# Kernel optimization log

Hardware: AMD Instinct MI355X
Metric: run time of the kernel (lower is better)

Reference implementation:

```python
import jax, jax.numpy as jnp
import numpy as np

DIM = 128
HEADS = 8
DH = DIM // HEADS
WIN = (4, 4, 4)
TOPK = 4
EPS = 1e-6


def _ln(x, g, b):
    mu = jnp.mean(x, -1, keepdims=True)
    var = jnp.mean((x - mu) ** 2, -1, keepdims=True)
    return (x - mu) * jax.lax.rsqrt(var + EPS) * g + b


def _win3d(x, p1, p2, p3):
    # x: [B,S,H,W,C] -> [B, p1*p2*p3, Ms, Mh, Mw, C]
    B, S, H, W, C = x.shape
    Ms, Mh, Mw = S // p1, H // p2, W // p3
    x = x.reshape(B, p1, Ms, p2, Mh, p3, Mw, C)
    x = x.transpose(0, 1, 3, 5, 2, 4, 6, 7)
    return x.reshape(B, p1 * p2 * p3, Ms, Mh, Mw, C)


def setup_inputs() -> dict:
    key = jax.random.key(0)
    ks = jax.random.split(key, 20)

    def lin(k, din, dout):
        return jax.random.normal(k, (din, dout), jnp.float32) * 0.02

    return {
        "x_in": jax.random.normal(ks[0], (2, 128, 16, 32, 32), jnp.float32),
        "x_g_in": jax.random.normal(ks[1], (2, 128, 8, 16, 16), jnp.float32),
        # Atten (global branch)
        "qkv_w": lin(ks[2], DIM, 3 * DIM), "qkv_b": jnp.zeros((3 * DIM,), jnp.float32),
        "proj_w": lin(ks[3], DIM, DIM), "proj_b": jnp.zeros((DIM,), jnp.float32),
        # shared LayerNorm (self.norm1 is reused everywhere in the original)
        "ln_g": jnp.ones((DIM,), jnp.float32), "ln_b": jnp.zeros((DIM,), jnp.float32),
        # mlp (global branch FFN)
        "mlp_w1": lin(ks[4], DIM, 4 * DIM), "mlp_b1": jnp.zeros((4 * DIM,), jnp.float32),
        "mlp_w2": lin(ks[5], 4 * DIM, DIM), "mlp_b2": jnp.zeros((DIM,), jnp.float32),
        # TopkRouting
        "rq_w": lin(ks[6], DIM, DIM), "rq_b": jnp.zeros((DIM,), jnp.float32),
        "rk_w": lin(ks[7], DIM, DIM), "rk_b": jnp.zeros((DIM,), jnp.float32),
        # fused qkv over concatenated local+gathered-global tokens
        "gqkv_w": lin(ks[8], DIM, 3 * DIM), "gqkv_b": jnp.zeros((3 * DIM,), jnp.float32),
        "wo_w": lin(ks[9], DIM, DIM), "wo_b": jnp.zeros((DIM,), jnp.float32),
        # mlp2 (local branch FFN)
        "mlp2_w1": lin(ks[10], DIM, 4 * DIM), "mlp2_b1": jnp.zeros((4 * DIM,), jnp.float32),
        "mlp2_w2": lin(ks[11], 4 * DIM, DIM), "mlp2_b2": jnp.zeros((DIM,), jnp.float32),
    }


def reference(x_in, x_g_in, qkv_w, qkv_b, proj_w, proj_b, ln_g, ln_b,
              mlp_w1, mlp_b1, mlp_w2, mlp_b2, rq_w, rq_b, rk_w, rk_b,
              gqkv_w, gqkv_b, wo_w, wo_b, mlp2_w1, mlp2_b1, mlp2_w2, mlp2_b2):
    B, C, S, H, W = x_in.shape
    Ms, Mh, Mw = WIN
    p1, p2, p3 = S // Ms, H // Mh, W // Mw  # pads are zero for these shapes
    nw, w3l = p1 * p2 * p3, Ms * Mh * Mw
    scale = DIM ** -0.5  # BiLevelRoutingAttention.scale = dim**-0.5 (not per-head)

    x = jnp.transpose(x_in, (0, 2, 3, 4, 1))  # [B,S,H,W,C]
    shortcut_l = _win3d(x, p1, p2, p3).reshape(B, nw, w3l, C)

    # ---- global branch: full self-attention + FFN ----
    _, _, gS, gH, gW = x_g_in.shape
    gN = gS * gH * gW
    xg = jnp.transpose(x_g_in, (0, 2, 3, 4, 1)).reshape(B, gN, C)
    h = _ln(xg, ln_g, ln_b)
    qkv = (h @ qkv_w + qkv_b).reshape(B, gN, 3, HEADS, DH).transpose(2, 0, 3, 1, 4)
    q, k, v = qkv[0], qkv[1], qkv[2]
    a = jax.nn.softmax(jnp.einsum('bhnd,bhmd->bhnm', q, k) * DH ** -0.5, axis=-1)
    o = jnp.einsum('bhnm,bhmd->bhnd', a, v).transpose(0, 2, 1, 3).reshape(B, gN, C)
    xg = (o @ proj_w + proj_b) + xg
    xg4 = xg.reshape(B, gS, gH, gW, C)
    h = _ln(xg4, ln_g, ln_b)
    xg4 = xg4 + (jax.nn.gelu(h @ mlp_w1 + mlp_b1, approximate=False) @ mlp_w2 + mlp_b2)

    # ---- top-k window routing ----
    swg = _win3d(xg4, p1, p2, p3)  # [B,nw,gMs,gMh,gMw,C]
    w3g = swg.shape[2] * swg.shape[3] * swg.shape[4]
    g_win = swg.mean((2, 3, 4))  # [B,nw,C]
    qh = g_win @ rq_w + rq_b
    kh = g_win @ rk_w + rk_b
    logit = jnp.einsum('bnc,bmc->bnm', qh * scale, kh)
    _tvals, tidx = jax.lax.top_k(logit, TOPK)  # r_weight is computed but unused in the original forward

    # gather top-k global windows' tokens per local window
    gflat = swg.reshape(B, nw, w3g, C)
    gath = jax.vmap(lambda kv, idx: kv[idx])(gflat, tidx)  # [B,nw,topk,w3g,C]
    sc = jnp.concatenate([shortcut_l, gath.reshape(B, nw, TOPK * w3g, C)], axis=2)
    w3 = w3l + TOPK * w3g

    # ---- local+routed attention over concatenated tokens ----
    qkvp = _ln(sc, ln_g, ln_b) @ gqkv_w + gqkv_b
    qp, kp, vp = jnp.split(qkvp, 3, axis=-1)
    qp = qp.reshape(B, nw, w3, HEADS, DH)
    kp = kp.reshape(B, nw, w3, HEADS, DH)
    vp = vp.reshape(B, nw, w3, HEADS, DH)
    aw = jax.nn.softmax(jnp.einsum('bnqhd,bnkhd->bnhqk', qp * scale, kp), axis=-1)
    out = jnp.einsum('bnhqk,bnkhd->bnqhd', aw, vp).reshape(B, nw, w3, C)

    l = out[:, :, :w3l] @ wo_w + wo_b + shortcut_l
    l = l.reshape(B, p1, p2, p3, Ms, Mh, Mw, C).transpose(0, 1, 4, 2, 5, 3, 6, 7).reshape(B, S, H, W, C)
    l = l + (jax.nn.gelu(_ln(l, ln_g, ln_b) @ mlp2_w1 + mlp2_b1, approximate=False) @ mlp2_w2 + mlp2_b2)

    l_out = jnp.transpose(l, (0, 4, 1, 2, 3))
    g_out = jnp.transpose(xg4, (0, 4, 1, 2, 3))
    return (l_out, g_out)
```

## Files before the change

### kernel.cpp

```cpp
#include <hip/hip_runtime.h>
#include <hip/hip_bf16.h>
#include <math.h>

#define BATCH 2
#define CDIM 128
#define SS 16
#define HH_ 32
#define WW_ 32
#define NSP (SS*HH_*WW_)
#define GS 8
#define GH 16
#define GW 16
#define GN (GS*GH*GW)
#define HEADS 8
#define DH 16
#define NW 256
#define W3L 64
#define W3G 8
#define TOPK 4
#define W3 (W3L + TOPK*W3G)
#define LN_EPS 1e-6f
#define ROUTE_SCALE 0.08838834764831845f
#define GATTN_SCALE 0.25f

typedef short bshort8 __attribute__((ext_vector_type(8)));
typedef float f32x4 __attribute__((ext_vector_type(4)));

__device__ __forceinline__ unsigned short f2bf(float f) {
    unsigned int u = __float_as_uint(f);
    unsigned int r = (u + 0x7fffu + ((u >> 16) & 1u)) >> 16;
    return (unsigned short)r;
}
__device__ __forceinline__ float gelu_exact(float x) {
    return 0.5f * x * (1.0f + erff(x * 0.70710678118654752f));
}
__device__ __forceinline__ float shfl_sum32(float v) {
#pragma unroll
    for (int m = 16; m > 0; m >>= 1) v += __shfl_xor(v, m);
    return v;
}
__device__ __forceinline__ float shfl_sum16(float v) {
#pragma unroll
    for (int m = 8; m > 0; m >>= 1) v += __shfl_xor(v, m);
    return v;
}
__device__ __forceinline__ float shfl_sum8(float v) {
#pragma unroll
    for (int m = 4; m > 0; m >>= 1) v += __shfl_xor(v, m);
    return v;
}

__global__ __launch_bounds__(256) void k_wprep_all(const float* __restrict__ gqkv_w,
        const float* __restrict__ m2_w1, const float* __restrict__ m2_w2,
        const float* __restrict__ proj_w, const float* __restrict__ mlp_w1,
        const float* __restrict__ mlp_w2, const float* __restrict__ wo_w,
        const float* __restrict__ qkv_w,
        unsigned short* __restrict__ wt, unsigned short* __restrict__ w1t,
        unsigned short* __restrict__ w2t, unsigned short* __restrict__ projt,
        unsigned short* __restrict__ gw1t, unsigned short* __restrict__ gw2t,
        unsigned short* __restrict__ wot, unsigned short* __restrict__ qkvt) {
    int id = blockIdx.x * 256 + threadIdx.x;
    if (id < 49152) {
        int n = id >> 7, k = id & 127;
        float v = gqkv_w[k * 384 + n];
        if (n < 128) v *= ROUTE_SCALE;
        wt[id] = f2bf(v);
    } else if (id < 114688) {
        int i = id - 49152; int n = i >> 7, k = i & 127;
        w1t[i] = f2bf(m2_w1[k * 512 + n]);
    } else if (id < 180224) {
        int i = id - 114688; int n = i >> 9, k = i & 511;
        w2t[i] = f2bf(m2_w2[k * 128 + n]);
    } else if (id < 196608) {
        int i = id - 180224; int n = i >> 7, k = i & 127;
        projt[i] = f2bf(proj_w[k * 128 + n]);
    } else if (id < 262144) {
        int i = id - 196608; int n = i >> 7, k = i & 127;
        gw1t[i] = f2bf(mlp_w1[k * 512 + n]);
    } else if (id < 327680) {
        int i = id - 262144; int n = i >> 9, k = i & 511;
        gw2t[i] = f2bf(mlp_w2[k * 128 + n]);
    } else if (id < 344064) {
        int i = id - 327680; int n = i >> 7, k = i & 127;
        wot[i] = f2bf(wo_w[k * 128 + n]);
    } else {
        int i = id - 344064; int n = i >> 7, k = i & 127;
        float v = qkv_w[k * 384 + n];
        if (n < 128) v *= GATTN_SCALE;
        qkvt[i] = f2bf(v);
    }
}

__global__ __launch_bounds__(256) void k_gqkv_mfma(const float* __restrict__ xg_in,
        const unsigned short* __restrict__ qkvt, const float* __restrict__ qkv_b,
        const float* __restrict__ ln_g, const float* __restrict__ ln_b,
        float* __restrict__ xg, unsigned short* __restrict__ qgb,
        unsigned short* __restrict__ kgb, unsigned short* __restrict__ vgtb) {
    int blk = blockIdx.x; int b = blk >> 7; int n0 = (blk & 127) * 16;
    int t = threadIdx.x; int w = t >> 6; int lane = t & 63;
    int l15 = lane & 15, quad = lane >> 4;
    __shared__ __align__(16) float xs[16 * 132];
    __shared__ __align__(16) unsigned short h[16 * 136];
    f32x4 zero4 = {0.f, 0.f, 0.f, 0.f};

    {
        int c = t >> 1, j0 = (t & 1) * 8;
        const float* src = xg_in + ((size_t)(b * 128 + c)) * GN + n0 + j0;
        float4 v0 = *(const float4*)src;
        float4 v1 = *(const float4*)(src + 4);
        xs[(j0 + 0) * 132 + c] = v0.x; xs[(j0 + 1) * 132 + c] = v0.y;
        xs[(j0 + 2) * 132 + c] = v0.z; xs[(j0 + 3) * 132 + c] = v0.w;
        xs[(j0 + 4) * 132 + c] = v1.x; xs[(j0 + 5) * 132 + c] = v1.y;
        xs[(j0 + 6) * 132 + c] = v1.z; xs[(j0 + 7) * 132 + c] = v1.w;
    }
    __syncthreads();
    {
        int j = t >> 4, p = t & 15, c0 = p * 8;
        float vv[8]; float s1 = 0.f;
#pragma unroll
        for (int i = 0; i < 8; i++) { vv[i] = xs[j * 132 + c0 + i]; s1 += vv[i]; }
        s1 = shfl_sum16(s1);
        float mu = s1 * (1.0f / 128.0f);
        float s2 = 0.f;
#pragma unroll
        for (int i = 0; i < 8; i++) { float d = vv[i] - mu; s2 += d * d; }
        s2 = shfl_sum16(s2);
        float rs = rsqrtf(s2 * (1.0f / 128.0f) + LN_EPS);
        float* dst = xg + ((size_t)(b * GN) + n0 + j) * 128 + c0;
        *(float4*)dst = *(float4*)&vv[0];
        *(float4*)(dst + 4) = *(float4*)&vv[4];
        unsigned short hb[8];
#pragma unroll
        for (int i4 = 0; i4 < 2; i4++) {
            float4 g4 = *(const float4*)(ln_g + c0 + i4 * 4);
            float4 b4 = *(const float4*)(ln_b + c0 + i4 * 4);
            hb[i4 * 4 + 0] = f2bf((vv[i4 * 4 + 0] - mu) * rs * g4.x + b4.x);
            hb[i4 * 4 + 1] = f2bf((vv[i4 * 4 + 1] - mu) * rs * g4.y + b4.y);
            hb[i4 * 4 + 2] = f2bf((vv[i4 * 4 + 2] - mu) * rs * g4.z + b4.z);
            hb[i4 * 4 + 3] = f2bf((vv[i4 * 4 + 3] - mu) * rs * g4.w + b4.w);
        }
        *(ushort4*)&h[j * 136 + c0] = *(ushort4*)&hb[0];
        *(ushort4*)&h[j * 136 + c0 + 4] = *(ushort4*)&hb[4];
    }
    __syncthreads();

    bshort8 a[4];
#pragma unroll
    for (int ks = 0; ks < 4; ks++)
        a[ks] = *(const bshort8*)(h + l15 * 136 + ks * 32 + quad * 8);
    int bh_base = b * HEADS;
#pragma unroll
    for (int part = 0; part < 2; part++) {
#pragma unroll
        for (int which = 0; which < 2; which++) {
            int nt = 2 * w + which;
            int ncol = part * 128 + nt * 16;
            f32x4 acc = zero4;
#pragma unroll
            for (int ks = 0; ks < 4; ks++) {
                bshort8 bfr = *(const bshort8*)(qkvt + (size_t)(ncol + l15) * 128 + ks * 32 + quad * 8);
                acc = __builtin_amdgcn_mfma_f32_16x16x32_bf16(a[ks], bfr, acc, 0, 0, 0);
            }
            float bias = qkv_b[ncol + l15] * (part == 0 ? GATTN_SCALE : 1.f);
            unsigned short* dst = (part == 0) ? qgb : kgb;
#pragma unroll
            for (int r = 0; r < 4; r++)
                dst[((size_t)(bh_base + nt) * GN + n0 + quad * 4 + r) * DH + l15] = f2bf(acc[r] + bias);
        }
    }
#pragma unroll
    for (int which = 0; which < 2; which++) {
        int mtv = 2 * w + which;
        f32x4 acc = zero4;
#pragma unroll
        for (int ks = 0; ks < 4; ks++) {
            bshort8 aw = *(const bshort8*)(qkvt + (size_t)(256 + mtv * 16 + l15) * 128 + ks * 32 + quad * 8);
            acc = __builtin_amdgcn_mfma_f32_16x16x32_bf16(aw, a[ks], acc, 0, 0, 0);
        }
#pragma unroll
        for (int r = 0; r < 4; r++) {
            float bias = qkv_b[256 + mtv * 16 + quad * 4 + r];
            vgtb[((size_t)(bh_base + mtv) * DH + quad * 4 + r) * GN + n0 + l15] = f2bf(acc[r] + bias);
        }
    }
}

__global__ __launch_bounds__(256) void k_gattn_mfma(const unsigned short* __restrict__ qgb,
        const unsigned short* __restrict__ kgb, const unsigned short* __restrict__ vgtb,
        float* __restrict__ og) {
    int blk = blockIdx.x;
    int bh = blk >> 7; int qt = (blk & 127) << 4;
    int b = bh >> 3, hh = bh & 7;
    int t = threadIdx.x; int w = t >> 6; int lane = t & 63;
    int col = lane & 15, quad = lane >> 4;
    __shared__ __align__(16) unsigned short Pbuf[4 * 16 * 40];
    __shared__ float po[4][64][4];
    __shared__ float pl[4][64][4];

    bshort8 aq = {0, 0, 0, 0, 0, 0, 0, 0};
    if (quad < 2)
        aq = *(const bshort8*)(qgb + ((size_t)bh * GN + qt + col) * DH + quad * 8);

    f32x4 o = {0.f, 0.f, 0.f, 0.f};
    float lsum[4] = {0.f, 0.f, 0.f, 0.f};
    const unsigned short* kb = kgb + (size_t)bh * GN * DH;
    const unsigned short* vb = vgtb + (size_t)bh * DH * GN;
    unsigned short* pb = Pbuf + w * (16 * 40);
    int row0 = quad * 4;
    int kbeg = w * 512;
    for (int kc = kbeg; kc < kbeg + 512; kc += 32) {
        bshort8 bk0 = {0, 0, 0, 0, 0, 0, 0, 0};
        bshort8 bk1 = {0, 0, 0, 0, 0, 0, 0, 0};
        if (quad < 2) {
            bk0 = *(const bshort8*)(kb + (size_t)(kc + col) * DH + quad * 8);
            bk1 = *(const bshort8*)(kb + (size_t)(kc + 16 + col) * DH + quad * 8);
        }
        f32x4 z = {0.f, 0.f, 0.f, 0.f};
        f32x4 s0 = __builtin_amdgcn_mfma_f32_16x16x32_bf16(aq, bk0, z, 0, 0, 0);
        f32x4 s1 = __builtin_amdgcn_mfma_f32_16x16x32_bf16(aq, bk1, z, 0, 0, 0);
        float p0[4], p1[4];
#pragma unroll
        for (int r = 0; r < 4; r++) {
            p0[r] = __expf(s0[r]); p1[r] = __expf(s1[r]);
            lsum[r] += p0[r] + p1[r];
        }
#pragma unroll
        for (int r = 0; r < 4; r++) {
            pb[(row0 + r) * 40 + col] = f2bf(p0[r]);
            pb[(row0 + r) * 40 + 16 + col] = f2bf(p1[r]);
        }
        bshort8 pA = *(const bshort8*)(pb + col * 40 + quad * 8);
        bshort8 bv = *(const bshort8*)(vb + (size_t)col * GN + kc + quad * 8);
        o = __builtin_amdgcn_mfma_f32_16x16x32_bf16(pA, bv, o, 0, 0, 0);
    }
#pragma unroll
    for (int r = 0; r < 4; r++) {
        float v = lsum[r];
        v += __shfl_xor(v, 1); v += __shfl_xor(v, 2);
        v += __shfl_xor(v, 4); v += __shfl_xor(v, 8);
        lsum[r] = v;
    }
#pragma unroll
    for (int r = 0; r < 4; r++) { po[w][lane][r] = o[r]; pl[w][lane][r] = lsum[r]; }
    __syncthreads();
    if (w == 0) {
#pragma unroll
        for (int r = 0; r < 4; r++) {
            float os = po[0][lane][r] + po[1][lane][r] + po[2][lane][r] + po[3][lane][r];
            float ls = pl[0][lane][r] + pl[1][lane][r] + pl[2][lane][r] + pl[3][lane][r];
            og[((size_t)(b * GN) + qt + quad * 4 + r) * 128 + hh * 16 + col] = os / ls;
        }
    }
}

__global__ __launch_bounds__(256) void k_gmlp_mfma(const float* __restrict__ og,
        const float* __restrict__ xg,
        const unsigned short* __restrict__ projt, const float* __restrict__ proj_b,
        const float* __restrict__ ln_g, const float* __restrict__ ln_b,
        const unsigned short* __restrict__ gw1t, const float* __restrict__ b1,
        const unsigned short* __restrict__ gw2t, const float* __restrict__ b2,
        float* __restrict__ xg4, float* __restrict__ gout) {
    int blk = blockIdx.x; int b = blk >> 7; int n0g = (blk & 127) * 16;
    int t = threadIdx.x; int w = t >> 6; int lane = t & 63;
    int l15 = lane & 15, quad = lane >> 4;
    __shared__ __align__(16) unsigned short ao[16 * 136];
    __shared__ __align__(16) float xs[16 * 132];
    __shared__ __align__(16) unsigned short h[16 * 136];
    __shared__ __align__(16) unsigned short h1[16 * 520];
    float* of32 = (float*)h1;
    f32x4 zero4 = {0.f, 0.f, 0.f, 0.f};

    {
        int j = t >> 4, p = t & 15, c0 = p * 8;
        size_t base = ((size_t)(b * GN) + n0g + j) * 128 + c0;
        float4 v0 = *(const float4*)(og + base);
        float4 v1 = *(const float4*)(og + base + 4);
        ushort4 u0 = { f2bf(v0.x), f2bf(v0.y), f2bf(v0.z), f2bf(v0.w) };
        ushort4 u1 = { f2bf(v1.x), f2bf(v1.y), f2bf(v1.z), f2bf(v1.w) };
        *(ushort4*)&ao[j * 136 + c0] = u0;
        *(ushort4*)&ao[j * 136 + c0 + 4] = u1;
        *(float4*)&xs[j * 132 + c0] = *(const float4*)(xg + base);
        *(float4*)&xs[j * 132 + c0 + 4] = *(const float4*)(xg + base + 4);
    }
    __syncthreads();

    {
        bshort8 a[4];
#pragma unroll
        for (int ks = 0; ks < 4; ks++)
            a[ks] = *(const bshort8*)(ao + l15 * 136 + ks * 32 + quad * 8);
#pragma unroll
        for (int nt = 0; nt < 2; nt++) {
            int n0 = w * 32 + nt * 16;
            f32x4 acc = zero4;
#pragma unroll
            for (int ks = 0; ks < 4; ks++) {
                bshort8 bfr = *(const bshort8*)(projt + (n0 + l15) * 128 + ks * 32 + quad * 8);
                acc = __builtin_amdgcn_mfma_f32_16x16x32_bf16(a[ks], bfr, acc, 0, 0, 0);
            }
            float bias = proj_b[n0 + l15];
#pragma unroll
            for (int r = 0; r < 4; r++) {
                int m = quad * 4 + r;
                xs[m * 132 + n0 + l15] += acc[r] + bias;
            }
        }
    }
    __syncthreads();

    {
        int j = t >> 4, p = t & 15, c0 = p * 8;
        float vv[8]; float s1 = 0.f;
#pragma unroll
        for (int i = 0; i < 8; i++) { vv[i] = xs[j * 132 + c0 + i]; s1 += vv[i]; }
        s1 = shfl_sum16(s1);
        float mu = s1 * (1.0f / 128.0f);
        float s2 = 0.f;
#pragma unroll
        for (int i = 0; i < 8; i++) { float d = vv[i] - mu; s2 += d * d; }
        s2 = shfl_sum16(s2);
        float rs = rsqrtf(s2 * (1.0f / 128.0f) + LN_EPS);
        unsigned short hb[8];
#pragma unroll
        for (int i4 = 0; i4 < 2; i4++) {
            float4 g4 = *(const float4*)(ln_g + c0 + i4 * 4);
            float4 b4 = *(const float4*)(ln_b + c0 + i4 * 4);
            hb[i4 * 4 + 0] = f2bf((vv[i4 * 4 + 0] - mu) * rs * g4.x + b4.x);
            hb[i4 * 4 + 1] = f2bf((vv[i4 * 4 + 1] - mu) * rs * g4.y + b4.y);
            hb[i4 * 4 + 2] = f2bf((vv[i4 * 4 + 2] - mu) * rs * g4.z + b4.z);
            hb[i4 * 4 + 3] = f2bf((vv[i4 * 4 + 3] - mu) * rs * g4.w + b4.w);
        }
        *(ushort4*)&h[j * 136 + c0] = *(ushort4*)&hb[0];
        *(ushort4*)&h[j * 136 + c0 + 4] = *(ushort4*)&hb[4];
    }
    __syncthreads();

    {
        bshort8 a[4];
#pragma unroll
        for (int ks = 0; ks < 4; ks++)
            a[ks] = *(const bshort8*)(h + l15 * 136 + ks * 32 + quad * 8);
#pragma unroll
        for (int nt = 0; nt < 8; nt++) {
            int n0 = w * 128 + nt * 16;
            f32x4 acc = zero4;
#pragma unroll
            for (int ks = 0; ks < 4; ks++) {
                bshort8 bfr = *(const bshort8*)(gw1t + (size_t)(n0 + l15) * 128 + ks * 32 + quad * 8);
                acc = __builtin_amdgcn_mfma_f32_16x16x32_bf16(a[ks], bfr, acc, 0, 0, 0);
            }
            float bias = b1[n0 + l15];
#pragma unroll
            for (int r = 0; r < 4; r++)
                h1[(quad * 4 + r) * 520 + n0 + l15] = f2bf(gelu_exact(acc[r] + bias));
        }
    }
    __syncthreads();

    f32x4 acc2[2]; acc2[0] = zero4; acc2[1] = zero4;
#pragma unroll 4
    for (int ks = 0; ks < 16; ks++) {
        bshort8 a = *(const bshort8*)(h1 + l15 * 520 + ks * 32 + quad * 8);
#pragma unroll
        for (int nt = 0; nt < 2; nt++) {
            int n0 = w * 32 + nt * 16;
            bshort8 bfr = *(const bshort8*)(gw2t + (size_t)(n0 + l15) * 512 + ks * 32 + quad * 8);
            acc2[nt] = __builtin_amdgcn_mfma_f32_16x16x32_bf16(a, bfr, acc2[nt], 0, 0, 0);
        }
    }
    __syncthreads();

    {
#pragma unroll
        for (int nt = 0; nt < 2; nt++) {
            int n0 = w * 32 + nt * 16;
            float bias = b2[n0 + l15];
#pragma unroll
            for (int r = 0; r < 4; r++) {
                int m = quad * 4 + r;
                float ov = xs[m * 132 + n0 + l15] + acc2[nt][r] + bias;
                of32[m * 132 + n0 + l15] = ov;
                xg4[((size_t)(b * GN) + n0g + m) * 128 + n0 + l15] = ov;
            }
        }
    }
    __syncthreads();

    {
        int cw = t >> 1, hf = t & 1, j0 = hf * 8;
        float* dst = gout + ((size_t)(b * 128 + cw)) * GN + n0g + j0;
#pragma unroll
        for (int i4 = 0; i4 < 2; i4++) {
            float4 ov = { of32[(j0 + i4 * 4 + 0) * 132 + cw], of32[(j0 + i4 * 4 + 1) * 132 + cw],
                          of32[(j0 + i4 * 4 + 2) * 132 + cw], of32[(j0 + i4 * 4 + 3) * 132 + cw] };
            *(float4*)(dst + i4 * 4) = ov;
        }
    }
}

__global__ void k_routing_qk(const float* __restrict__ xg4,
                             const float* __restrict__ rq_w, const float* __restrict__ rq_b,
                             const float* __restrict__ rk_w, const float* __restrict__ rk_b,
                             float* __restrict__ qh, float* __restrict__ kh) {
    int wid = blockIdx.x; int b = wid / NW, n = wid % NW;
    int c = threadIdx.x;
    int i1 = n / 64, i2 = (n / 8) % 8, i3 = n % 8;
    __shared__ float g[CDIM];
    float s = 0.f;
#pragma unroll
    for (int j = 0; j < W3G; j++) {
        int ds = j >> 2, dh = (j >> 1) & 1, dw = j & 1;
        int gi = ((i1 * 2 + ds) * GH + (i2 * 2 + dh)) * GW + (i3 * 2 + dw);
        s += xg4[((size_t)(b * GN + gi)) * CDIM + c];
    }
    g[c] = s * (1.0f / W3G);
    __syncthreads();
    float aq = rq_b[c], ak = rk_b[c];
    for (int k = 0; k < CDIM; k++) { float gv = g[k]; aq = fmaf(gv, rq_w[k * CDIM + c], aq); ak = fmaf(gv, rk_w[k * CDIM + c], ak); }
    qh[(size_t)wid * CDIM + c] = aq;
    kh[(size_t)wid * CDIM + c] = ak;
}

__global__ void k_topk(const float* __restrict__ qh, const float* __restrict__ kh,
                       int* __restrict__ tidx) {
    int wid = blockIdx.x; int b = wid / NW;
    int m = threadIdx.x;
    __shared__ float q[CDIM];
    __shared__ float lv[NW];
    __shared__ int li[NW];
    if (m < CDIM) q[m] = qh[(size_t)wid * CDIM + m] * ROUTE_SCALE;
    __syncthreads();
    float acc = 0.f;
    const float* kr = kh + ((size_t)b * NW + m) * CDIM;
    for (int k = 0; k < CDIM; k++) acc = fmaf(q[k], kr[k], acc);
#pragma unroll
    for (int sel = 0; sel < TOPK; sel++) {
        lv[m] = acc; li[m] = m; __syncthreads();
#pragma unroll
        for (int s = 128; s > 0; s >>= 1) {
            if (m < s) {
                if (lv[m + s] > lv[m] || (lv[m + s] == lv[m] && li[m + s] < li[m])) {
                    lv[m] = lv[m + s]; li[m] = li[m + s];
                }
            }
            __syncthreads();
        }
        int best = li[0]; __syncthreads();
        if (m == best) acc = -1e30f;
        if (m == 0) tidx[wid * TOPK + sel] = best;
    }
}

__global__ __launch_bounds__(256) void k_lnsc_local(const float* __restrict__ x_in,
        const float* __restrict__ ln_g, const float* __restrict__ ln_b,
        unsigned short* __restrict__ lnsc) {
    int blk = blockIdx.x;
    int wt = blk & 1; int hh = (blk >> 1) & 31; int s = (blk >> 6) & 15; int b = blk >> 10;
    int w0 = wt * 16;
    int t = threadIdx.x;
    __shared__ float tile[16][132];
    {
        int c = t >> 1; int wq = (t & 1) * 8;
        const float* src = x_in + (((size_t)(b * 128 + c) * SS + s)) * 1024 + hh * 32 + w0 + wq;
        float4 v0 = *(const float4*)src;
        float4 v1 = *(const float4*)(src + 4);
        tile[wq + 0][c] = v0.x; tile[wq + 1][c] = v0.y; tile[wq + 2][c] = v0.z; tile[wq + 3][c] = v0.w;
        tile[wq + 4][c] = v1.x; tile[wq + 5][c] = v1.y; tile[wq + 6][c] = v1.z; tile[wq + 7][c] = v1.w;
    }
    __syncthreads();
    int w = t >> 4; int j = t & 15;
    float vals[8];
    float s1 = 0.f;
#pragma unroll
    for (int i = 0; i < 8; i++) { vals[i] = tile[w][j * 8 + i]; s1 += vals[i]; }
    s1 = shfl_sum16(s1);
    float mu = s1 * (1.0f / 128.0f);
    float s2 = 0.f;
#pragma unroll
    for (int i = 0; i < 8; i++) { float d = vals[i] - mu; s2 += d * d; }
    s2 = shfl_sum16(s2);
    float rs = rsqrtf(s2 * (1.0f / 128.0f) + LN_EPS);
    float4 g0 = *(const float4*)(ln_g + j * 8);
    float4 g1 = *(const float4*)(ln_g + j * 8 + 4);
    float4 b0 = *(const float4*)(ln_b + j * 8);
    float4 b1 = *(const float4*)(ln_b + j * 8 + 4);
    float gv[8] = { g0.x, g0.y, g0.z, g0.w, g1.x, g1.y, g1.z, g1.w };
    float bv[8] = { b0.x, b0.y, b0.z, b0.w, b1.x, b1.y, b1.z, b1.w };
    int ww = w0 + w;
    int n = (s >> 2) * 64 + (hh >> 2) * 8 + (ww >> 2);
    int slot = (s & 3) * 16 + (hh & 3) * 4 + (ww & 3);
    unsigned short* dst = lnsc + ((size_t)(b * NW + n) * W3 + slot) * 128 + j * 8;
    ushort4 u0, u1;
    u0.x = f2bf((vals[0] - mu) * rs * gv[0] + bv[0]);
    u0.y = f2bf((vals[1] - mu) * rs * gv[1] + bv[1]);
    u0.z = f2bf((vals[2] - mu) * rs * gv[2] + bv[2]);
    u0.w = f2bf((vals[3] - mu) * rs * gv[3] + bv[3]);
    u1.x = f2bf((vals[4] - mu) * rs * gv[4] + bv[4]);
    u1.y = f2bf((vals[5] - mu) * rs * gv[5] + bv[5]);
    u1.z = f2bf((vals[6] - mu) * rs * gv[6] + bv[6]);
    u1.w = f2bf((vals[7] - mu) * rs * gv[7] + bv[7]);
    *(ushort4*)dst = u0;
    *(ushort4*)(dst + 4) = u1;
}

__global__ __launch_bounds__(256) void k_lnsc_gath(const float* __restrict__ xg4,
        const int* __restrict__ tidx,
        const float* __restrict__ ln_g, const float* __restrict__ ln_b,
        unsigned short* __restrict__ lnsc) {
    int blk = blockIdx.x;
    int kk = blk & 3; int wn = blk >> 2;
    int b = wn >> 8;
    int g = tidx[wn * TOPK + kk];
    int gi1 = g >> 6, gi2 = (g >> 3) & 7, gi3 = g & 7;
    int t = threadIdx.x; int j = t >> 5, lj = t & 31;
    int ds = j >> 2, dh = (j >> 1) & 1, dw = j & 1;
    int gi = ((gi1 * 2 + ds) * GH + (gi2 * 2 + dh)) * GW + (gi3 * 2 + dw);
    float4 v = *(const float4*)(xg4 + ((size_t)(b * GN + gi)) * 128 + lj * 4);
    float s1 = shfl_sum32(v.x + v.y + v.z + v.w);
    float mu = s1 * (1.0f / 128.0f);
    float d0 = v.x - mu, d1 = v.y - mu, d2 = v.z - mu, d3 = v.w - mu;
    float s2 = shfl_sum32(d0 * d0 + d1 * d1 + d2 * d2 + d3 * d3);
    float rs = rsqrtf(s2 * (1.0f / 128.0f) + LN_EPS);
    float4 g4 = *(const float4*)(ln_g + lj * 4);
    float4 b4 = *(const float4*)(ln_b + lj * 4);
    ushort4 u;
    u.x = f2bf(d0 * rs * g4.x + b4.x);
    u.y = f2bf(d1 * rs * g4.y + b4.y);
    u.z = f2bf(d2 * rs * g4.z + b4.z);
    u.w = f2bf(d3 * rs * g4.w + b4.w);
    *(ushort4*)(lnsc + ((size_t)wn * W3 + 64 + kk * 8 + j) * 128 + lj * 4) = u;
}

__global__ __launch_bounds__(512, 4) void k_local_mfma(const unsigned short* __restrict__ lnsc,
        const unsigned short* __restrict__ wt, const float* __restrict__ gqkv_b,
        float* __restrict__ aout) {
    int wn = blockIdx.x;
    int t = threadIdx.x; int w = t >> 6; int lane = t & 63;
    int l15 = lane & 15, quad = lane >> 4;
    __shared__ __align__(16) unsigned short Qs[64 * 136];
    __shared__ __align__(16) unsigned short Ks2[96 * 136];
    __shared__ __align__(16) unsigned short Vts[128 * 104];
    __shared__ __align__(16) unsigned short Ps[8][16 * 40];

    const unsigned short* Xb = lnsc + (size_t)wn * W3 * 128;
    f32x4 zero4 = {0.f, 0.f, 0.f, 0.f};

    bshort8 qw[4], kw[4], vw[4];
#pragma unroll
    for (int ks = 0; ks < 4; ks++) {
        qw[ks] = *(const bshort8*)(wt + (w * 16 + l15) * 128 + ks * 32 + quad * 8);
        kw[ks] = *(const bshort8*)(wt + (128 + w * 16 + l15) * 128 + ks * 32 + quad * 8);
        vw[ks] = *(const bshort8*)(wt + (256 + w * 16 + l15) * 128 + ks * 32 + quad * 8);
    }
    float qbias = gqkv_b[w * 16 + l15] * ROUTE_SCALE;
    float kbias = gqkv_b[128 + w * 16 + l15];
    float vbias[4];
#pragma unroll
    for (int r = 0; r < 4; r++) vbias[r] = gqkv_b[256 + w * 16 + quad * 4 + r];

    for (int mt = 0; mt < 6; mt++) {
        bshort8 a[4];
#pragma unroll
        for (int ks = 0; ks < 4; ks++)
            a[ks] = *(const bshort8*)(Xb + (mt * 16 + l15) * 128 + ks * 32 + quad * 8);
        f32x4 acck = zero4;
        f32x4 accv = zero4;
#pragma unroll
        for (int ks = 0; ks < 4; ks++) {
            acck = __builtin_amdgcn_mfma_f32_16x16x32_bf16(a[ks], kw[ks], acck, 0, 0, 0);
            accv = __builtin_amdgcn_mfma_f32_16x16x32_bf16(vw[ks], a[ks], accv, 0, 0, 0);
        }
#pragma unroll
        for (int r = 0; r < 4; r++) {
            Ks2[(mt * 16 + quad * 4 + r) * 136 + w * 16 + l15] = f2bf(acck[r] + kbias);
            Vts[(w * 16 + quad * 4 + r) * 104 + mt * 16 + l15] = f2bf(accv[r] + vbias[r]);
        }
        if (mt < 4) {
            f32x4 accq = zero4;
#pragma unroll
            for (int ks = 0; ks < 4; ks++)
                accq = __builtin_amdgcn_mfma_f32_16x16x32_bf16(a[ks], qw[ks], accq, 0, 0, 0);
#pragma unroll
            for (int r = 0; r < 4; r++)
                Qs[(mt * 16 + quad * 4 + r) * 136 + w * 16 + l15] = f2bf(accq[r] + qbias);
        }
    }

    unsigned short* Pw = &Ps[w][0];
    bshort8 zfrag = {0, 0, 0, 0, 0, 0, 0, 0};
    int h = w;
    for (int mt = 0; mt < 4; mt++) {
        bshort8 aq = zfrag;
        if (quad < 2)
            aq = *(const bshort8*)(Qs + (mt * 16 + l15) * 136 + h * 16 + quad * 8);
        float rsum[4] = {0.f, 0.f, 0.f, 0.f};
        f32x4 oacc = zero4;
#pragma unroll
        for (int kc = 0; kc < 96; kc += 32) {
#pragma unroll
            for (int sub = 0; sub < 2; sub++) {
                int nt = (kc >> 4) + sub;
                bshort8 bk = zfrag;
                if (quad < 2)
                    bk = *(const bshort8*)(Ks2 + (nt * 16 + l15) * 136 + h * 16 + quad * 8);
                f32x4 s = __builtin_amdgcn_mfma_f32_16x16x32_bf16(aq, bk, zero4, 0, 0, 0);
#pragma unroll
                for (int r = 0; r < 4; r++) {
                    float p = __expf(s[r]);
                    rsum[r] += p;
                    Pw[(quad * 4 + r) * 40 + sub * 16 + l15] = f2bf(p);
                }
            }
            bshort8 ap = *(const bshort8*)(Pw + l15 * 40 + quad * 8);
            bshort8 bv = *(const bshort8*)(Vts + (h * 16 + l15) * 104 + kc + quad * 8);
            oacc = __builtin_amdgcn_mfma_f32_16x16x32_bf16(ap, bv, oacc, 0, 0, 0);
        }
#pragma unroll
        for (int r = 0; r < 4; r++) {
            float v = rsum[r];
            v += __shfl_xor(v, 1); v += __shfl_xor(v, 2);
            v += __shfl_xor(v, 4); v += __shfl_xor(v, 8);
            rsum[r] = v;
        }
#pragma unroll
        for (int r = 0; r < 4; r++)
            aout[((size_t)wn * W3L + mt * 16 + quad * 4 + r) * 128 + h * 16 + l15]
                = oacc[r] / rsum[r];
    }
}

__global__ __launch_bounds__(256) void k_wo_mfma(const float* __restrict__ aout,
        const unsigned short* __restrict__ wot, const float* __restrict__ wo_b,
        const float* __restrict__ x_in, float* __restrict__ lpre) {
    int blk = blockIdx.x; int T0 = blk * 32;
    int b = T0 >> 14; int sp0 = T0 & 16383;
    int t = threadIdx.x; int w = t >> 6; int lane = t & 63;
    int l15 = lane & 15, quad = lane >> 4;
    __shared__ __align__(16) unsigned short as2[32 * 136];
    __shared__ __align__(16) float xs[32 * 132];
    f32x4 zero4 = {0.f, 0.f, 0.f, 0.f};

    {
        int j = t >> 3, p = t & 7, c0 = p * 16;
        int sp = sp0 + j;
        int s = sp >> 10, hh = (sp >> 5) & 31, ww = sp & 31;
        int n = (s >> 2) * 64 + (hh >> 2) * 8 + (ww >> 2);
        int slot = (s & 3) * 16 + (hh & 3) * 4 + (ww & 3);
        const float* src = aout + (((size_t)(b * NW + n)) * W3L + slot) * 128 + c0;
#pragma unroll
        for (int i4 = 0; i4 < 4; i4++) {
            float4 v = *(const float4*)(src + i4 * 4);
            ushort4 u = { f2bf(v.x), f2bf(v.y), f2bf(v.z), f2bf(v.w) };
            *(ushort4*)&as2[j * 136 + c0 + i4 * 4] = u;
        }
    }
    {
        int c = t >> 1, half = t & 1, j0 = half * 16;
        const float* src = x_in + ((size_t)(b * 128 + c)) * 16384 + sp0 + j0;
#pragma unroll
        for (int i4 = 0; i4 < 4; i4++) {
            float4 v = *(const float4*)(src + i4 * 4);
            xs[(j0 + i4 * 4 + 0) * 132 + c] = v.x;
            xs[(j0 + i4 * 4 + 1) * 132 + c] = v.y;
            xs[(j0 + i4 * 4 + 2) * 132 + c] = v.z;
            xs[(j0 + i4 * 4 + 3) * 132 + c] = v.w;
        }
    }
    __syncthreads();

    bshort8 a[2][4];
#pragma unroll
    for (int mt = 0; mt < 2; mt++)
#pragma unroll
        for (int ks = 0; ks < 4; ks++)
            a[mt][ks] = *(const bshort8*)(as2 + (mt * 16 + l15) * 136 + ks * 32 + quad * 8);
#pragma unroll
    for (int nt = 0; nt < 2; nt++) {
        int n0 = w * 32 + nt * 16;
        f32x4 acc0 = zero4, acc1 = zero4;
#pragma unroll
        for (int ks = 0; ks < 4; ks++) {
            bshort8 bfr = *(const bshort8*)(wot + (n0 + l15) * 128 + ks * 32 + quad * 8);
            acc0 = __builtin_amdgcn_mfma_f32_16x16x32_bf16(a[0][ks], bfr, acc0, 0, 0, 0);
            acc1 = __builtin_amdgcn_mfma_f32_16x16x32_bf16(a[1][ks], bfr, acc1, 0, 0, 0);
        }
        float bias = wo_b[n0 + l15];
#pragma unroll
        for (int r = 0; r < 4; r++) {
            int m0 = quad * 4 + r;
            int m1 = 16 + quad * 4 + r;
            lpre[((size_t)T0 + m0) * 128 + n0 + l15] = acc0[r] + bias + xs[m0 * 132 + n0 + l15];
            lpre[((size_t)T0 + m1) * 128 + n0 + l15] = acc1[r] + bias + xs[m1 * 132 + n0 + l15];
        }
    }
}

__global__ __launch_bounds__(256) void k_mlp2_mfma(const float* __restrict__ lpre,
        const float* __restrict__ ln_g, const float* __restrict__ ln_b,
        const unsigned short* __restrict__ w1t, const float* __restrict__ b1,
        const unsigned short* __restrict__ w2t, const float* __restrict__ b2,
        float* __restrict__ lout) {
    int blk = blockIdx.x;
    int T0 = blk * 32;
    int b = T0 >> 14;
    int sp = T0 & 16383;
    int t = threadIdx.x; int w = t >> 6; int lane = t & 63;
    int l15 = lane & 15, quad = lane >> 4;
    __shared__ __align__(16) unsigned short buf[32 * 520];
    float* of32 = (float*)buf;

    {
        int j = t >> 3, p = t & 7, c0 = p * 16;
        const float* src = lpre + ((size_t)T0 + j) * 128 + c0;
        float4 v0 = *(const float4*)(src + 0);
        float4 v1 = *(const float4*)(src + 4);
        float4 v2 = *(const float4*)(src + 8);
        float4 v3 = *(const float4*)(src + 12);
        float s1 = (v0.x + v0.y + v0.z + v0.w) + (v1.x + v1.y + v1.z + v1.w)
                 + (v2.x + v2.y + v2.z + v2.w) + (v3.x + v3.y + v3.z + v3.w);
        s1 = shfl_sum8(s1);
        float mu = s1 * (1.0f / 128.0f);
        float vv[16] = { v0.x, v0.y, v0.z, v0.w, v1.x, v1.y, v1.z, v1.w,
                         v2.x, v2.y, v2.z, v2.w, v3.x, v3.y, v3.z, v3.w };
        float s2 = 0.f;
#pragma unroll
        for (int i = 0; i < 16; i++) { float d = vv[i] - mu; s2 += d * d; }
        s2 = shfl_sum8(s2);
        float rs = rsqrtf(s2 * (1.0f / 128.0f) + LN_EPS);
        unsigned short hb[16];
#pragma unroll
        for (int i4 = 0; i4 < 4; i4++) {
            float4 g4 = *(const float4*)(ln_g + c0 + i4 * 4);
            float4 b4 = *(const float4*)(ln_b + c0 + i4 * 4);
            hb[i4 * 4 + 0] = f2bf((vv[i4 * 4 + 0] - mu) * rs * g4.x + b4.x);
            hb[i4 * 4 + 1] = f2bf((vv[i4 * 4 + 1] - mu) * rs * g4.y + b4.y);
            hb[i4 * 4 + 2] = f2bf((vv[i4 * 4 + 2] - mu) * rs * g4.z + b4.z);
            hb[i4 * 4 + 3] = f2bf((vv[i4 * 4 + 3] - mu) * rs * g4.w + b4.w);
        }
        *(ushort4*)&buf[j * 136 + c0 + 0] = *(ushort4*)&hb[0];
        *(ushort4*)&buf[j * 136 + c0 + 4] = *(ushort4*)&hb[4];
        *(ushort4*)&buf[j * 136 + c0 + 8] = *(ushort4*)&hb[8];
        *(ushort4*)&buf[j * 136 + c0 + 12] = *(ushort4*)&hb[12];
    }
    __syncthreads();

    bshort8 a1[2][4];
#pragma unroll
    for (int mt = 0; mt < 2; mt++)
#pragma unroll
        for (int ks = 0; ks < 4; ks++)
            a1[mt][ks] = *(const bshort8*)(buf + (mt * 16 + l15) * 136 + ks * 32 + quad * 8);
    __syncthreads();

    f32x4 zero4 = {0.f, 0.f, 0.f, 0.f};
    {
        int n0w = w * 128;
#pragma unroll
        for (int nt = 0; nt < 8; nt++) {
            int n0 = n0w + nt * 16;
            f32x4 acc0 = zero4, acc1 = zero4;
#pragma unroll
            for (int ks = 0; ks < 4; ks++) {
                bshort8 bfr = *(const bshort8*)(w1t + (size_t)(n0 + l15) * 128 + ks * 32 + quad * 8);
                acc0 = __builtin_amdgcn_mfma_f32_16x16x32_bf16(a1[0][ks], bfr, acc0, 0, 0, 0);
                acc1 = __builtin_amdgcn_mfma_f32_16x16x32_bf16(a1[1][ks], bfr, acc1, 0, 0, 0);
            }
            float bias = b1[n0 + l15];
#pragma unroll
            for (int r = 0; r < 4; r++) {
                buf[(quad * 4 + r) * 520 + n0 + l15] = f2bf(gelu_exact(acc0[r] + bias));
                buf[(16 + quad * 4 + r) * 520 + n0 + l15] = f2bf(gelu_exact(acc1[r] + bias));
            }
        }
    }
    __syncthreads();

    f32x4 acc[2][2];
    acc[0][0] = zero4; acc[0][1] = zero4; acc[1][0] = zero4; acc[1][1] = zero4;
    {
#pragma unroll 4
        for (int ks = 0; ks < 16; ks++) {
            bshort8 a0 = *(const bshort8*)(buf + (l15) * 520 + ks * 32 + quad * 8);
            bshort8 a1b = *(const bshort8*)(buf + (16 + l15) * 520 + ks * 32 + quad * 8);
#pragma unroll
            for (int nt = 0; nt < 2; nt++) {
                int n0 = w * 32 + nt * 16;
                bshort8 bfr = *(const bshort8*)(w2t + (size_t)(n0 + l15) * 512 + ks * 32 + quad * 8);
                acc[0][nt] = __builtin_amdgcn_mfma_f32_16x16x32_bf16(a0, bfr, acc[0][nt], 0, 0, 0);
                acc[1][nt] = __builtin_amdgcn_mfma_f32_16x16x32_bf16(a1b, bfr, acc[1][nt], 0, 0, 0);
            }
        }
    }
    __syncthreads();

#pragma unroll
    for (int mt = 0; mt < 2; mt++) {
#pragma unroll
        for (int nt = 0; nt < 2; nt++) {
            int n0 = w * 32 + nt * 16;
            float bias = b2[n0 + l15];
#pragma unroll
            for (int r = 0; r < 4; r++) {
                int m = mt * 16 + quad * 4 + r;
                float res = lpre[((size_t)T0 + m) * 128 + n0 + l15];
                of32[m * 132 + n0 + l15] = res + acc[mt][nt][r] + bias;
            }
        }
    }
    __syncthreads();

    {
        int c = t >> 1, half = t & 1, j0 = half * 16;
        float* dst = lout + ((size_t)(b * 128 + c)) * NSP + sp + j0;
#pragma unroll
        for (int i4 = 0; i4 < 4; i4++) {
            float4 ov = { of32[(j0 + i4 * 4 + 0) * 132 + c], of32[(j0 + i4 * 4 + 1) * 132 + c],
                          of32[(j0 + i4 * 4 + 2) * 132 + c], of32[(j0 + i4 * 4 + 3) * 132 + c] };
            *(float4*)(dst + i4 * 4) = ov;
        }
    }
}

extern "C" void kernel_launch(void* const* d_in, const int* in_sizes, int n_in,
                              void* d_out, int out_size, void* d_ws, size_t ws_size,
                              hipStream_t stream) {
    const float* x_in   = (const float*)d_in[0];
    const float* xg_in  = (const float*)d_in[1];
    const float* qkv_w  = (const float*)d_in[2];
    const float* qkv_b  = (const float*)d_in[3];
    const float* proj_w = (const float*)d_in[4];
    const float* proj_b = (const float*)d_in[5];
    const float* ln_g   = (const float*)d_in[6];
    const float* ln_b   = (const float*)d_in[7];
    const float* mlp_w1 = (const float*)d_in[8];
    const float* mlp_b1 = (const float*)d_in[9];
    const float* mlp_w2 = (const float*)d_in[10];
    const float* mlp_b2 = (const float*)d_in[11];
    const float* rq_w   = (const float*)d_in[12];
    const float* rq_b   = (const float*)d_in[13];
    const float* rk_w   = (const float*)d_in[14];
    const float* rk_b   = (const float*)d_in[15];
    const float* gqkv_w = (const float*)d_in[16];
    const float* gqkv_b = (const float*)d_in[17];
    const float* wo_w   = (const float*)d_in[18];
    const float* wo_b   = (const float*)d_in[19];
    const float* m2_w1  = (const float*)d_in[20];
    const float* m2_b1  = (const float*)d_in[21];
    const float* m2_w2  = (const float*)d_in[22];
    const float* m2_b2  = (const float*)d_in[23];

    float* out = (float*)d_out;
    float* ws  = (float*)d_ws;

    float* xg4 = ws;
    float* xg  = ws + 524288;
    unsigned short* qgb  = (unsigned short*)(ws + 1048576);
    unsigned short* kgb  = (unsigned short*)(ws + 1310720);
    unsigned short* vgtb = (unsigned short*)(ws + 1572864);
    float* og  = ws + 1835008;
    float* qh  = ws + 2359296;
    float* kh  = ws + 2424832;
    int*   tidx = (int*)(ws + 2490368);
    unsigned short* lnsc = (unsigned short*)(ws + 2492416);
    float* aout = ws + 2492416 + 3145728;
    float* lpre = ws + 9832448;
    unsigned short* wt   = (unsigned short*)(ws + 14026752);
    unsigned short* w1t  = (unsigned short*)(ws + 14051328);
    unsigned short* w2t  = (unsigned short*)(ws + 14084096);
    unsigned short* projt = (unsigned short*)(ws + 14116864);
    unsigned short* gw1t  = (unsigned short*)(ws + 14125056);
    unsigned short* gw2t  = (unsigned short*)(ws + 14157824);
    unsigned short* wot   = (unsigned short*)(ws + 14190592);
    unsigned short* qkvt  = (unsigned short*)(ws + 14198784);

    const size_t L_OUT = (size_t)BATCH * CDIM * NSP;
    float* gout = out + L_OUT;

    hipLaunchKernelGGL(k_wprep_all, dim3(1536), dim3(256), 0, stream,
                       gqkv_w, m2_w1, m2_w2, proj_w, mlp_w1, mlp_w2, wo_w, qkv_w,
                       wt, w1t, w2t, projt, gw1t, gw2t, wot, qkvt);
    hipLaunchKernelGGL(k_gqkv_mfma, dim3(256), dim3(256), 0, stream,
                       xg_in, qkvt, qkv_b, ln_g, ln_b, xg, qgb, kgb, vgtb);
    hipLaunchKernelGGL(k_gattn_mfma, dim3(2048), dim3(256), 0, stream, qgb, kgb, vgtb, og);
    hipLaunchKernelGGL(k_gmlp_mfma, dim3(256), dim3(256), 0, stream,
                       og, xg, projt, proj_b, ln_g, ln_b, gw1t, mlp_b1, gw2t, mlp_b2,
                       xg4, gout);
    hipLaunchKernelGGL(k_routing_qk, dim3(512), dim3(128), 0, stream,
                       xg4, rq_w, rq_b, rk_w, rk_b, qh, kh);
    hipLaunchKernelGGL(k_topk, dim3(512), dim3(256), 0, stream, qh, kh, tidx);
    hipLaunchKernelGGL(k_lnsc_local, dim3(2048), dim3(256), 0, stream,
                       x_in, ln_g, ln_b, lnsc);
    hipLaunchKernelGGL(k_lnsc_gath, dim3(2048), dim3(256), 0, stream,
                       xg4, tidx, ln_g, ln_b, lnsc);
    hipLaunchKernelGGL(k_local_mfma, dim3(512), dim3(512), 0, stream,
                       lnsc, wt, gqkv_b, aout);
    hipLaunchKernelGGL(k_wo_mfma, dim3(1024), dim3(256), 0, stream,
                       aout, wot, wo_b, x_in, lpre);
    hipLaunchKernelGGL(k_mlp2_mfma, dim3(1024), dim3(256), 0, stream,
                       lpre, ln_g, ln_b, w1t, m2_b1, w2t, m2_b2, out);
}
```

Baseline: 268.6 us.

## Pre-swizzle bf16 weights into MFMA fragment order, fast GELU, prefetch residual

Weight prep now writes every bf16 weight matrix in per-lane MFMA fragment order, so each lane's B-operand load in the GEMM kernels is a fully contiguous 16-byte access instead of a strided row read. The prep kernel also runs with fewer threads, each converting 8 elements. Exact erf-based GELU is swapped for the Abramowitz-Stegun polynomial with __expf, which adds a small approximation error. The residual values in the local MLP kernel are loaded into registers at kernel start instead of during the epilogue.

```diff
diff --git a/kernel.cpp b/kernel.cpp
--- a/kernel.cpp
+++ b/kernel.cpp
@@ -32,7 +32,15 @@
     return (unsigned short)r;
 }
 __device__ __forceinline__ float gelu_exact(float x) {
-    return 0.5f * x * (1.0f + erff(x * 0.70710678118654752f));
+    float z = x * 0.70710678118654752f;
+    float az = fabsf(z);
+    float t = 1.0f / fmaf(0.3275911f, az, 1.0f);
+    float poly = t * fmaf(t, fmaf(t, fmaf(t, fmaf(t, 1.061405429f, -1.453152027f),
+                     1.421413741f), -0.284496736f), 0.254829592f);
+    float e = __expf(-az * az);
+    float erfv = 1.0f - poly * e;
+    erfv = (z < 0.f) ? -erfv : erfv;
+    return 0.5f * x * (1.0f + erfv);
 }
 __device__ __forceinline__ float shfl_sum32(float v) {
 #pragma unroll
@@ -60,35 +68,28 @@
         unsigned short* __restrict__ gw1t, unsigned short* __restrict__ gw2t,
         unsigned short* __restrict__ wot, unsigned short* __restrict__ qkvt) {
     int id = blockIdx.x * 256 + threadIdx.x;
-    if (id < 49152) {
-        int n = id >> 7, k = id & 127;
-        float v = gqkv_w[k * 384 + n];
-        if (n < 128) v *= ROUTE_SCALE;
-        wt[id] = f2bf(v);
-    } else if (id < 114688) {
-        int i = id - 49152; int n = i >> 7, k = i & 127;
-        w1t[i] = f2bf(m2_w1[k * 512 + n]);
-    } else if (id < 180224) {
-        int i = id - 114688; int n = i >> 9, k = i & 511;
-        w2t[i] = f2bf(m2_w2[k * 128 + n]);
-    } else if (id < 196608) {
-        int i = id - 180224; int n = i >> 7, k = i & 127;
-        projt[i] = f2bf(proj_w[k * 128 + n]);
-    } else if (id < 262144) {
-        int i = id - 196608; int n = i >> 7, k = i & 127;
-        gw1t[i] = f2bf(mlp_w1[k * 512 + n]);
-    } else if (id < 327680) {
-        int i = id - 262144; int n = i >> 9, k = i & 511;
-        gw2t[i] = f2bf(mlp_w2[k * 128 + n]);
-    } else if (id < 344064) {
-        int i = id - 327680; int n = i >> 7, k = i & 127;
-        wot[i] = f2bf(wo_w[k * 128 + n]);
-    } else {
-        int i = id - 344064; int n = i >> 7, k = i & 127;
-        float v = qkv_w[k * 384 + n];
-        if (n < 128) v *= GATTN_SCALE;
-        qkvt[i] = f2bf(v);
-    }
+    int frag = id >> 6, lane = id & 63;
+    int l15 = lane & 15, quad = lane >> 4;
+    const float* srcw; unsigned short* dstw; int KS, OUT, lf; float sc = 1.f;
+    if (frag < 96)        { lf = frag;       srcw = gqkv_w; dstw = wt;    KS = 4;  OUT = 384; if ((lf >> 2) < 8) sc = ROUTE_SCALE; }
+    else if (frag < 224)  { lf = frag - 96;  srcw = m2_w1;  dstw = w1t;   KS = 4;  OUT = 512; }
+    else if (frag < 352)  { lf = frag - 224; srcw = m2_w2;  dstw = w2t;   KS = 16; OUT = 128; }
+    else if (frag < 384)  { lf = frag - 352; srcw = proj_w; dstw = projt; KS = 4;  OUT = 128; }
+    else if (frag < 512)  { lf = frag - 384; srcw = mlp_w1; dstw = gw1t;  KS = 4;  OUT = 512; }
+    else if (frag < 640)  { lf = frag - 512; srcw = mlp_w2; dstw = gw2t;  KS = 16; OUT = 128; }
+    else if (frag < 672)  { lf = frag - 640; srcw = wo_w;   dstw = wot;   KS = 4;  OUT = 128; }
+    else                  { lf = frag - 672; srcw = qkv_w;  dstw = qkvt;  KS = 4;  OUT = 384; if ((lf >> 2) < 8) sc = GATTN_SCALE; }
+    int ksh = (KS == 16) ? 4 : 2;
+    int tile = lf >> ksh, ks = lf & (KS - 1);
+    int n = tile * 16 + l15;
+    int k0 = ks * 32 + quad * 8;
+    const float* s = srcw + (size_t)k0 * OUT + n;
+    unsigned short o[8];
+#pragma unroll
+    for (int e = 0; e < 8; e++) o[e] = f2bf(s[(size_t)e * OUT] * sc);
+    unsigned short* d = dstw + ((size_t)lf * 64 + lane) * 8;
+    *(ushort4*)d = *(ushort4*)&o[0];
+    *(ushort4*)(d + 4) = *(ushort4*)&o[4];
 }
 
 __global__ __launch_bounds__(256) void k_gqkv_mfma(const float* __restrict__ xg_in,
@@ -154,13 +155,13 @@
 #pragma unroll
         for (int which = 0; which < 2; which++) {
             int nt = 2 * w + which;
+            f32x4 acc = zero4;
+#pragma unroll
+            for (int ks = 0; ks < 4; ks++) {
+                bshort8 bfr = *(const bshort8*)(qkvt + (((size_t)(part * 8 + nt) * 4 + ks) * 64 + lane) * 8);
+                acc = __builtin_amdgcn_mfma_f32_16x16x32_bf16(a[ks], bfr, acc, 0, 0, 0);
+            }
             int ncol = part * 128 + nt * 16;
-            f32x4 acc = zero4;
-#pragma unroll
-            for (int ks = 0; ks < 4; ks++) {
-                bshort8 bfr = *(const bshort8*)(qkvt + (size_t)(ncol + l15) * 128 + ks * 32 + quad * 8);
-                acc = __builtin_amdgcn_mfma_f32_16x16x32_bf16(a[ks], bfr, acc, 0, 0, 0);
-            }
             float bias = qkv_b[ncol + l15] * (part == 0 ? GATTN_SCALE : 1.f);
             unsigned short* dst = (part == 0) ? qgb : kgb;
 #pragma unroll
@@ -174,7 +175,7 @@
         f32x4 acc = zero4;
 #pragma unroll
         for (int ks = 0; ks < 4; ks++) {
-            bshort8 aw = *(const bshort8*)(qkvt + (size_t)(256 + mtv * 16 + l15) * 128 + ks * 32 + quad * 8);
+            bshort8 aw = *(const bshort8*)(qkvt + (((size_t)(16 + mtv) * 4 + ks) * 64 + lane) * 8);
             acc = __builtin_amdgcn_mfma_f32_16x16x32_bf16(aw, a[ks], acc, 0, 0, 0);
         }
 #pragma unroll
@@ -291,13 +292,13 @@
             a[ks] = *(const bshort8*)(ao + l15 * 136 + ks * 32 + quad * 8);
 #pragma unroll
         for (int nt = 0; nt < 2; nt++) {
+            f32x4 acc = zero4;
+#pragma unroll
+            for (int ks = 0; ks < 4; ks++) {
+                bshort8 bfr = *(const bshort8*)(projt + (((size_t)(w * 2 + nt) * 4 + ks) * 64 + lane) * 8);
+                acc = __builtin_amdgcn_mfma_f32_16x16x32_bf16(a[ks], bfr, acc, 0, 0, 0);
+            }
             int n0 = w * 32 + nt * 16;
-            f32x4 acc = zero4;
-#pragma unroll
-            for (int ks = 0; ks < 4; ks++) {
-                bshort8 bfr = *(const bshort8*)(projt + (n0 + l15) * 128 + ks * 32 + quad * 8);
-                acc = __builtin_amdgcn_mfma_f32_16x16x32_bf16(a[ks], bfr, acc, 0, 0, 0);
-            }
             float bias = proj_b[n0 + l15];
 #pragma unroll
             for (int r = 0; r < 4; r++) {
@@ -342,13 +343,13 @@
             a[ks] = *(const bshort8*)(h + l15 * 136 + ks * 32 + quad * 8);
 #pragma unroll
         for (int nt = 0; nt < 8; nt++) {
+            f32x4 acc = zero4;
+#pragma unroll
+            for (int ks = 0; ks < 4; ks++) {
+                bshort8 bfr = *(const bshort8*)(gw1t + (((size_t)(w * 8 + nt) * 4 + ks) * 64 + lane) * 8);
+                acc = __builtin_amdgcn_mfma_f32_16x16x32_bf16(a[ks], bfr, acc, 0, 0, 0);
+            }
             int n0 = w * 128 + nt * 16;
-            f32x4 acc = zero4;
-#pragma unroll
-            for (int ks = 0; ks < 4; ks++) {
-                bshort8 bfr = *(const bshort8*)(gw1t + (size_t)(n0 + l15) * 128 + ks * 32 + quad * 8);
-                acc = __builtin_amdgcn_mfma_f32_16x16x32_bf16(a[ks], bfr, acc, 0, 0, 0);
-            }
             float bias = b1[n0 + l15];
 #pragma unroll
             for (int r = 0; r < 4; r++)
@@ -363,8 +364,7 @@
         bshort8 a = *(const bshort8*)(h1 + l15 * 520 + ks * 32 + quad * 8);
 #pragma unroll
         for (int nt = 0; nt < 2; nt++) {
-            int n0 = w * 32 + nt * 16;
-            bshort8 bfr = *(const bshort8*)(gw2t + (size_t)(n0 + l15) * 512 + ks * 32 + quad * 8);
+            bshort8 bfr = *(const bshort8*)(gw2t + (((size_t)(w * 2 + nt) * 16 + ks) * 64 + lane) * 8);
             acc2[nt] = __builtin_amdgcn_mfma_f32_16x16x32_bf16(a, bfr, acc2[nt], 0, 0, 0);
         }
     }
@@ -548,9 +548,9 @@
     bshort8 qw[4], kw[4], vw[4];
 #pragma unroll
     for (int ks = 0; ks < 4; ks++) {
-        qw[ks] = *(const bshort8*)(wt + (w * 16 + l15) * 128 + ks * 32 + quad * 8);
-        kw[ks] = *(const bshort8*)(wt + (128 + w * 16 + l15) * 128 + ks * 32 + quad * 8);
-        vw[ks] = *(const bshort8*)(wt + (256 + w * 16 + l15) * 128 + ks * 32 + quad * 8);
+        qw[ks] = *(const bshort8*)(wt + (((size_t)(0 + w) * 4 + ks) * 64 + lane) * 8);
+        kw[ks] = *(const bshort8*)(wt + (((size_t)(8 + w) * 4 + ks) * 64 + lane) * 8);
+        vw[ks] = *(const bshort8*)(wt + (((size_t)(16 + w) * 4 + ks) * 64 + lane) * 8);
     }
     float qbias = gqkv_b[w * 16 + l15] * ROUTE_SCALE;
     float kbias = gqkv_b[128 + w * 16 + l15];
@@ -680,7 +680,7 @@
         f32x4 acc0 = zero4, acc1 = zero4;
 #pragma unroll
         for (int ks = 0; ks < 4; ks++) {
-            bshort8 bfr = *(const bshort8*)(wot + (n0 + l15) * 128 + ks * 32 + quad * 8);
+            bshort8 bfr = *(const bshort8*)(wot + (((size_t)(w * 2 + nt) * 4 + ks) * 64 + lane) * 8);
             acc0 = __builtin_amdgcn_mfma_f32_16x16x32_bf16(a[0][ks], bfr, acc0, 0, 0, 0);
             acc1 = __builtin_amdgcn_mfma_f32_16x16x32_bf16(a[1][ks], bfr, acc1, 0, 0, 0);
         }
@@ -709,6 +709,15 @@
     __shared__ __align__(16) unsigned short buf[32 * 520];
     float* of32 = (float*)buf;
 
+    float res[2][2][4];
+#pragma unroll
+    for (int mt = 0; mt < 2; mt++)
+#pragma unroll
+        for (int nt = 0; nt < 2; nt++)
+#pragma unroll
+            for (int r = 0; r < 4; r++)
+                res[mt][nt][r] = lpre[((size_t)T0 + mt * 16 + quad * 4 + r) * 128 + w * 32 + nt * 16 + l15];
+
     {
         int j = t >> 3, p = t & 7, c0 = p * 16;
         const float* src = lpre + ((size_t)T0 + j) * 128 + c0;
@@ -754,14 +763,13 @@
 
     f32x4 zero4 = {0.f, 0.f, 0.f, 0.f};
     {
-        int n0w = w * 128;
 #pragma unroll
         for (int nt = 0; nt < 8; nt++) {
-            int n0 = n0w + nt * 16;
+            int n0 = w * 128 + nt * 16;
             f32x4 acc0 = zero4, acc1 = zero4;
 #pragma unroll
             for (int ks = 0; ks < 4; ks++) {
-                bshort8 bfr = *(const bshort8*)(w1t + (size_t)(n0 + l15) * 128 + ks * 32 + quad * 8);
+                bshort8 bfr = *(const bshort8*)(w1t + (((size_t)(w * 8 + nt) * 4 + ks) * 64 + lane) * 8);
                 acc0 = __builtin_amdgcn_mfma_f32_16x16x32_bf16(a1[0][ks], bfr, acc0, 0, 0, 0);
                 acc1 = __builtin_amdgcn_mfma_f32_16x16x32_bf16(a1[1][ks], bfr, acc1, 0, 0, 0);
             }
@@ -784,8 +792,7 @@
             bshort8 a1b = *(const bshort8*)(buf + (16 + l15) * 520 + ks * 32 + quad * 8);
 #pragma unroll
             for (int nt = 0; nt < 2; nt++) {
-                int n0 = w * 32 + nt * 16;
-                bshort8 bfr = *(const bshort8*)(w2t + (size_t)(n0 + l15) * 512 + ks * 32 + quad * 8);
+                bshort8 bfr = *(const bshort8*)(w2t + (((size_t)(w * 2 + nt) * 16 + ks) * 64 + lane) * 8);
                 acc[0][nt] = __builtin_amdgcn_mfma_f32_16x16x32_bf16(a0, bfr, acc[0][nt], 0, 0, 0);
                 acc[1][nt] = __builtin_amdgcn_mfma_f32_16x16x32_bf16(a1b, bfr, acc[1][nt], 0, 0, 0);
             }
@@ -802,8 +809,7 @@
 #pragma unroll
             for (int r = 0; r < 4; r++) {
                 int m = mt * 16 + quad * 4 + r;
-                float res = lpre[((size_t)T0 + m) * 128 + n0 + l15];
-                of32[m * 132 + n0 + l15] = res + acc[mt][nt][r] + bias;
+                of32[m * 132 + n0 + l15] = res[mt][nt][r] + acc[mt][nt][r] + bias;
             }
         }
     }
@@ -876,7 +882,7 @@
     const size_t L_OUT = (size_t)BATCH * CDIM * NSP;
     float* gout = out + L_OUT;
 
-    hipLaunchKernelGGL(k_wprep_all, dim3(1536), dim3(256), 0, stream,
+    hipLaunchKernelGGL(k_wprep_all, dim3(192), dim3(256), 0, stream,
                        gqkv_w, m2_w1, m2_w2, proj_w, mlp_w1, mlp_w2, wo_w, qkv_w,
                        wt, w1t, w2t, projt, gw1t, gw2t, wot, qkvt);
     hipLaunchKernelGGL(k_gqkv_mfma, dim3(256), dim3(256), 0, stream,
```

Result: faster. 248.0 us (-7.7%).
